# Kernel optimization log

Hardware: AMD Instinct MI355X
Metric: run time of the kernel (lower is better)

The kernel has to match this reference:

```python
import jax, jax.numpy as jnp
import numpy as np
from functools import partial

INPUT_SIZE = 24
HIDDEN = 64
NUM_LAYERS = 3
OUT_FEATURES = 4


def _lstm_layer(x, w_ih, w_hh, b_ih, b_hh):
    """Single LSTM layer, PyTorch gate order (i, f, g, o).
    x: [B, T, in] -> returns h sequence [B, T, H]."""
    B = x.shape[0]
    H = w_hh.shape[1]
    # Precompute input contribution for all timesteps: [B, T, 4H]
    gx = jnp.einsum('bti,gi->btg', x, w_ih) + b_ih + b_hh

    def step(carry, g_t):
        h, c = carry
        gates = g_t + h @ w_hh.T  # [B, 4H]
        i, f, g, o = jnp.split(gates, 4, axis=-1)
        i = jax.nn.sigmoid(i)
        f = jax.nn.sigmoid(f)
        g = jnp.tanh(g)
        o = jax.nn.sigmoid(o)
        c = f * c + i * g
        h = o * jnp.tanh(c)
        return (h, c), h

    h0 = jnp.zeros((B, H), dtype=x.dtype)
    c0 = jnp.zeros((B, H), dtype=x.dtype)
    (_, _), hs = jax.lax.scan(step, (h0, c0), jnp.swapaxes(gx, 0, 1))  # hs: [T, B, H]
    return jnp.swapaxes(hs, 0, 1)  # [B, T, H]


def setup_inputs() -> dict:
    key = jax.random.key(0)
    ks = jax.random.split(key, 16)
    B, T = 1024, 512
    inp = {"x": jax.random.normal(ks[0], (B, T, INPUT_SIZE), dtype=jnp.float32)}
    k = 1
    s = 1.0 / np.sqrt(HIDDEN)
    for layer in range(NUM_LAYERS):
        in_dim = INPUT_SIZE if layer == 0 else HIDDEN
        inp[f"w_ih_{layer}"] = jax.random.uniform(ks[k], (4 * HIDDEN, in_dim), minval=-s, maxval=s, dtype=jnp.float32); k += 1
        inp[f"w_hh_{layer}"] = jax.random.uniform(ks[k], (4 * HIDDEN, HIDDEN), minval=-s, maxval=s, dtype=jnp.float32); k += 1
        inp[f"b_ih_{layer}"] = jax.random.uniform(ks[k], (4 * HIDDEN,), minval=-s, maxval=s, dtype=jnp.float32); k += 1
        inp[f"b_hh_{layer}"] = jax.random.uniform(ks[k], (4 * HIDDEN,), minval=-s, maxval=s, dtype=jnp.float32); k += 1
    inp["w_lin"] = jax.random.uniform(ks[13], (OUT_FEATURES, HIDDEN), minval=-s, maxval=s, dtype=jnp.float32)
    inp["b_lin"] = jax.random.uniform(ks[14], (OUT_FEATURES,), minval=-s, maxval=s, dtype=jnp.float32)
    return inp


def reference(x, w_ih_0, w_hh_0, b_ih_0, b_hh_0,
              w_ih_1, w_hh_1, b_ih_1, b_hh_1,
              w_ih_2, w_hh_2, b_ih_2, b_hh_2,
              w_lin, b_lin):
    params = [(w_ih_0, w_hh_0, b_ih_0, b_hh_0),
              (w_ih_1, w_hh_1, b_ih_1, b_hh_1),
              (w_ih_2, w_hh_2, b_ih_2, b_hh_2)]
    h = x
    for (w_ih, w_hh, b_ih, b_hh) in params:  # fixed 3-layer stack
        h = _lstm_layer(h, w_ih, w_hh, b_ih, b_hh)
    last = h[:, -1]                      # [B, H]
    return last @ w_lin.T + b_lin        # [B, 4]
```

## Files before the change

### kernel.cpp

```cpp
#include <hip/hip_runtime.h>


typedef __attribute__((ext_vector_type(8))) _Float16 half8;
typedef __attribute__((ext_vector_type(4))) float floatx4;

static constexpr int T_STEPS = 512;

#define NL2E  (-1.4426950408889634f)
#define N2L2E (-2.8853900817779268f)

#define H_OFF0   0
#define H_OFF1   1024
#define H_OFF2   2048
#define SM_BYTES 3072

__device__ __forceinline__ floatx4 mfma16(half8 a, half8 b, floatx4 c) {
    return __builtin_amdgcn_mfma_f32_16x16x32_f16(a, b, c, 0, 0, 0);
}

__device__ __forceinline__ half8 cvt8s(const float* src, float s) {
    float4 v0 = *(const float4*)(src);
    float4 v1 = *(const float4*)(src + 4);
    half8 h;
    h[0] = (_Float16)(v0.x * s); h[1] = (_Float16)(v0.y * s);
    h[2] = (_Float16)(v0.z * s); h[3] = (_Float16)(v0.w * s);
    h[4] = (_Float16)(v1.x * s); h[5] = (_Float16)(v1.y * s);
    h[6] = (_Float16)(v1.z * s); h[7] = (_Float16)(v1.w * s);
    return h;
}

__device__ __forceinline__ void lds_barrier() {
    asm volatile("s_waitcnt lgkmcnt(0)" ::: "memory");
    __builtin_amdgcn_s_barrier();
}

__global__ __launch_bounds__(768, 3) void lstm3_v12(
    const float* __restrict__ x,
    const float* __restrict__ w_ih0, const float* __restrict__ w_hh0,
    const float* __restrict__ b_ih0, const float* __restrict__ b_hh0,
    const float* __restrict__ w_ih1, const float* __restrict__ w_hh1,
    const float* __restrict__ b_ih1, const float* __restrict__ b_hh1,
    const float* __restrict__ w_ih2, const float* __restrict__ w_hh2,
    const float* __restrict__ b_ih2, const float* __restrict__ b_hh2,
    const float* __restrict__ w_lin, const float* __restrict__ b_lin,
    float* __restrict__ out)
{
    __shared__ __align__(16) char sm[SM_BYTES];

    const int tid  = threadIdx.x;
    const int lane = tid & 63;
    const int wave = tid >> 6;
    const int L    = wave >> 2;
    const int w    = wave & 3;
    const int l15  = lane & 15;
    const int l4   = lane >> 4;
    const int bat  = l15 >> 2;
    const int b0   = blockIdx.x * 4;
    const int u    = w * 16 + l15;

    for (int i = tid; i < SM_BYTES / 16; i += 768)
        *(floatx4*)(&sm[i * 16]) = floatx4{0.f, 0.f, 0.f, 0.f};

    const float* wi = (L == 0) ? w_ih0 : (L == 1 ? w_ih1 : w_ih2);
    const float* wh = (L == 0) ? w_hh0 : (L == 1 ? w_hh1 : w_hh2);
    const float* bi = (L == 0) ? b_ih0 : (L == 1 ? b_ih1 : b_ih2);
    const float* bh = (L == 0) ? b_hh0 : (L == 1 ? b_hh1 : b_hh2);
    const int HB = (L == 0) ? H_OFF0 : (L == 1 ? H_OFF1 : H_OFF2);
    const int PB = (L == 1) ? H_OFF0 : H_OFF1;

    half8 wf[4][4];
#pragma unroll
    for (int tt = 0; tt < 4; ++tt) {
        const int g = tt * 64 + u;
        const float sc = (tt == 2) ? N2L2E : NL2E;
        if (L == 0) {
            half8 z;
#pragma unroll
            for (int j = 0; j < 8; ++j) z[j] = (_Float16)0.f;
            wf[tt][0] = (l4 < 3) ? cvt8s(w_ih0 + g * 24 + l4 * 8, sc) : z;
            wf[tt][1] = cvt8s(w_hh0 + g * 64 + l4 * 8, sc);
            wf[tt][2] = cvt8s(w_hh0 + g * 64 + 32 + l4 * 8, sc);
            wf[tt][3] = z;
        } else {
            wf[tt][0] = cvt8s(wi + g * 64 + l4 * 8, sc);
            wf[tt][1] = cvt8s(wi + g * 64 + 32 + l4 * 8, sc);
            wf[tt][2] = cvt8s(wh + g * 64 + l4 * 8, sc);
            wf[tt][3] = cvt8s(wh + g * 64 + 32 + l4 * 8, sc);
        }
    }
    floatx4 bv[4];
#pragma unroll
    for (int tt = 0; tt < 4; ++tt) {
        const float sc = (tt == 2) ? N2L2E : NL2E;
        float b = sc * (bi[tt * 64 + u] + bh[tt * 64 + u]);
        bv[tt][0] = b; bv[tt][1] = b; bv[tt][2] = b; bv[tt][3] = b;
    }
    const floatx4 Z4 = floatx4{0.f, 0.f, 0.f, 0.f};

    const int swzR = (bat & 1) << 5;
    int rb0 = 0, rb1 = 0, rb2 = 0, rb3 = 0;
    if (L == 0) {
        rb1 = H_OFF0 + ((bat * 128 + 0  + l4 * 16) ^ swzR);
        rb2 = H_OFF0 + ((bat * 128 + 64 + l4 * 16) ^ swzR);
    } else {
        rb0 = PB + ((bat * 128 + 0  + l4 * 16) ^ swzR);
        rb1 = PB + ((bat * 128 + 64 + l4 * 16) ^ swzR);
        rb2 = HB + ((bat * 128 + 0  + l4 * 16) ^ swzR);
        rb3 = HB + ((bat * 128 + 64 + l4 * 16) ^ swzR);
    }
    const int wb = HB + ((l4 * 128 + u * 2) ^ ((l4 & 1) << 5));

    const int par_e = L & 1;
    const int so_e = par_e * 512, sp_e = (par_e ^ 1) * 512;
    const int eA0 = rb0 + so_e;
    const int eA1 = rb1 + ((L == 0) ? sp_e : so_e);
    const int eA2 = rb2 + sp_e;
    const int eA3 = rb3 + sp_e;
    const int eWr = wb + so_e;
    const int oA0 = rb0 + sp_e;
    const int oA1 = rb1 + ((L == 0) ? so_e : sp_e);
    const int oA2 = rb2 + so_e;
    const int oA3 = rb3 + so_e;
    const int oWr = wb + sp_e;

    float4 xA0{0,0,0,0}, xA1{0,0,0,0}, xB0{0,0,0,0}, xB1{0,0,0,0};
    const bool xv = (L == 0) && (l4 < 3);
    const float* xpe = nullptr;
    const float* xpo = nullptr;
    if (xv) {
        const float* xb_ = x + (long)(b0 + bat) * T_STEPS * 24 + l4 * 8;
        xA0 = *(const float4*)(xb_);      xA1 = *(const float4*)(xb_ + 4);
        xB0 = *(const float4*)(xb_ + 24); xB1 = *(const float4*)(xb_ + 28);
        xpe = xb_ + 48;
        xpo = xb_ + 72;
    }

    float cst = 0.0f;
    __syncthreads();

    auto body = [&](int s, int A0, int A1, int A2, int A3, int WR)
        __attribute__((always_inline)) {
        const int t = s - L;
        const bool active = ((unsigned)t < (unsigned)T_STEPS);

        if (active) {
            float e0, e1, e2, e3;
            if (L == 0) {
                const float4 v0 = (t & 1) ? xB0 : xA0;
                const float4 v1 = (t & 1) ? xB1 : xA1;
                half8 aX;
                aX[0] = (_Float16)v0.x; aX[1] = (_Float16)v0.y;
                aX[2] = (_Float16)v0.z; aX[3] = (_Float16)v0.w;
                aX[4] = (_Float16)v1.x; aX[5] = (_Float16)v1.y;
                aX[6] = (_Float16)v1.z; aX[7] = (_Float16)v1.w;
                half8 a1 = *(const half8*)(&sm[A1]);
                half8 a2 = *(const half8*)(&sm[A2]);
#pragma unroll
                for (int tt = 0; tt < 4; ++tt) {
                    floatx4 accA = mfma16(aX, wf[tt][0], bv[tt]);
                    floatx4 accB = mfma16(a1, wf[tt][1], Z4);
                    accB = mfma16(a2, wf[tt][2], accB);
                    float e = __builtin_amdgcn_exp2f(accA[0] + accB[0]);
                    if (tt == 0) e0 = e; else if (tt == 1) e1 = e;
                    else if (tt == 2) e2 = e; else e3 = e;
                }
                if (xv && t + 2 < T_STEPS) {
                    if (t & 1) {
                        xB0 = *(const float4*)(xpo); xB1 = *(const float4*)(xpo + 4);
                        xpo += 48;
                    } else {
                        xA0 = *(const float4*)(xpe); xA1 = *(const float4*)(xpe + 4);
                        xpe += 48;
                    }
                }
            } else {
                half8 a0 = *(const half8*)(&sm[A0]);
                half8 a1 = *(const half8*)(&sm[A1]);
                half8 a2 = *(const half8*)(&sm[A2]);
                half8 a3 = *(const half8*)(&sm[A3]);
#pragma unroll
                for (int tt = 0; tt < 4; ++tt) {
                    floatx4 accA = mfma16(a0, wf[tt][0], bv[tt]);
                    floatx4 accB = mfma16(a2, wf[tt][2], Z4);
                    accA = mfma16(a1, wf[tt][1], accA);
                    accB = mfma16(a3, wf[tt][3], accB);
                    float e = __builtin_amdgcn_exp2f(accA[0] + accB[0]);
                    if (tt == 0) e0 = e; else if (tt == 1) e1 = e;
                    else if (tt == 2) e2 = e; else e3 = e;
                }
            }

            float ig = __builtin_amdgcn_rcpf(1.f + e0);
            float fg = __builtin_amdgcn_rcpf(1.f + e1);
            float sg = __builtin_amdgcn_rcpf(1.f + e2);
            float og = __builtin_amdgcn_rcpf(1.f + e3);
            float gg = fmaf(2.f, sg, -1.f);
            cst = fmaf(fg, cst, ig * gg);
            float et = __builtin_amdgcn_exp2f(cst * N2L2E);
            float th = fmaf(2.f, __builtin_amdgcn_rcpf(1.f + et), -1.f);
            float hv = og * th;
            *(_Float16*)(&sm[WR]) = (_Float16)hv;
        }
        lds_barrier();
    };

    for (int s = 0; s < T_STEPS + 2; s += 2) {
        body(s,     eA0, eA1, eA2, eA3, eWr);
        body(s + 1, oA0, oA1, oA2, oA3, oWr);
    }

    __syncthreads();

    if (tid < 16) {
        const int bb = tid >> 2, o = tid & 3;
        const int sl = ((T_STEPS - 1) & 1) * 512;
        float accum = b_lin[o];
#pragma unroll
        for (int k = 0; k < 64; ++k) {
            const int off = H_OFF2 + sl + ((bb * 128 + k * 2) ^ ((bb & 1) << 5));
            accum = fmaf((float)*(const _Float16*)(&sm[off]), w_lin[o * 64 + k], accum);
        }
        out[(b0 + bb) * 4 + o] = accum;
    }
}

extern "C" void kernel_launch(void* const* d_in, const int* in_sizes, int n_in,
                              void* d_out, int out_size, void* d_ws, size_t ws_size,
                              hipStream_t stream) {
    const float* x     = (const float*)d_in[0];
    const float* w_ih0 = (const float*)d_in[1];
    const float* w_hh0 = (const float*)d_in[2];
    const float* b_ih0 = (const float*)d_in[3];
    const float* b_hh0 = (const float*)d_in[4];
    const float* w_ih1 = (const float*)d_in[5];
    const float* w_hh1 = (const float*)d_in[6];
    const float* b_ih1 = (const float*)d_in[7];
    const float* b_hh1 = (const float*)d_in[8];
    const float* w_ih2 = (const float*)d_in[9];
    const float* w_hh2 = (const float*)d_in[10];
    const float* b_ih2 = (const float*)d_in[11];
    const float* b_hh2 = (const float*)d_in[12];
    const float* w_lin = (const float*)d_in[13];
    const float* b_lin = (const float*)d_in[14];

    lstm3_v12<<<dim3(256), dim3(768), 0, stream>>>(
        x, w_ih0, w_hh0, b_ih0, b_hh0,
        w_ih1, w_hh1, b_ih1, b_hh1,
        w_ih2, w_hh2, b_ih2, b_hh2,
        w_lin, b_lin, (float*)d_out);
}
```

Baseline: 310.2 us.

## Stage layer-0 inputs through double-buffered LDS and chain MFMA accumulators

Layer-0 input rows are now loaded cooperatively by a few lanes per wave, one timestep ahead, converted to fp16 and written into a double-buffered LDS region. The MFMA loop then reads a ready half8 operand instead of each lane holding its own float registers and converting them every step. This removes redundant per-lane global loads and conversions and frees registers. Separately, the split dual-accumulator MFMA chains are merged into one serial chain, which saves a vector add but lengthens the MFMA dependency chain.

```diff
diff --git a/kernel.cpp b/kernel.cpp
--- a/kernel.cpp
+++ b/kernel.cpp
@@ -2,6 +2,7 @@
 
 
 typedef __attribute__((ext_vector_type(8))) _Float16 half8;
+typedef __attribute__((ext_vector_type(4))) _Float16 half4;
 typedef __attribute__((ext_vector_type(4))) float floatx4;
 
 static constexpr int T_STEPS = 512;
@@ -9,10 +10,11 @@
 #define NL2E  (-1.4426950408889634f)
 #define N2L2E (-2.8853900817779268f)
 
-#define H_OFF0   0
-#define H_OFF1   1024
-#define H_OFF2   2048
-#define SM_BYTES 3072
+#define XOFF     0
+#define H_OFF0   512
+#define H_OFF1   1536
+#define H_OFF2   2560
+#define SM_BYTES 3584
 
 __device__ __forceinline__ floatx4 mfma16(half8 a, half8 b, floatx4 c) {
     return __builtin_amdgcn_mfma_f32_16x16x32_f16(a, b, c, 0, 0, 0);
@@ -34,7 +36,7 @@
     __builtin_amdgcn_s_barrier();
 }
 
-__global__ __launch_bounds__(768, 3) void lstm3_v12(
+__global__ __launch_bounds__(768, 3) void lstm3_v13(
     const float* __restrict__ x,
     const float* __restrict__ w_ih0, const float* __restrict__ w_hh0,
     const float* __restrict__ b_ih0, const float* __restrict__ b_hh0,
@@ -95,7 +97,6 @@
         float b = sc * (bi[tt * 64 + u] + bh[tt * 64 + u]);
         bv[tt][0] = b; bv[tt][1] = b; bv[tt][2] = b; bv[tt][3] = b;
     }
-    const floatx4 Z4 = floatx4{0.f, 0.f, 0.f, 0.f};
 
     const int swzR = (bat & 1) << 5;
     int rb0 = 0, rb1 = 0, rb2 = 0, rb3 = 0;
@@ -109,6 +110,9 @@
         rb3 = HB + ((bat * 128 + 64 + l4 * 16) ^ swzR);
     }
     const int wb = HB + ((l4 * 128 + u * 2) ^ ((l4 & 1) << 5));
+
+    const int xr0 = XOFF + bat * 64 + l4 * 16;
+    const int xr1 = xr0 + 256;
 
     const int par_e = L & 1;
     const int so_e = par_e * 512, sp_e = (par_e ^ 1) * 512;
@@ -123,55 +127,46 @@
     const int oA3 = rb3 + so_e;
     const int oWr = wb + sp_e;
 
-    float4 xA0{0,0,0,0}, xA1{0,0,0,0}, xB0{0,0,0,0}, xB1{0,0,0,0};
-    const bool xv = (L == 0) && (l4 < 3);
-    const float* xpe = nullptr;
-    const float* xpo = nullptr;
-    if (xv) {
-        const float* xb_ = x + (long)(b0 + bat) * T_STEPS * 24 + l4 * 8;
-        xA0 = *(const float4*)(xb_);      xA1 = *(const float4*)(xb_ + 4);
-        xB0 = *(const float4*)(xb_ + 24); xB1 = *(const float4*)(xb_ + 28);
-        xpe = xb_ + 48;
-        xpo = xb_ + 72;
+    const bool stg = (L == 0) && (lane < 6);
+    const int xf = lane;
+    const int sxw0 = XOFF + 0   + w * 64 + xf * 8;
+    const int sxw1 = XOFF + 256 + w * 64 + xf * 8;
+    const float* xg = nullptr;
+    if (stg) xg = x + ((long)(b0 + w) * T_STEPS + 1) * 24 + xf * 4;
+
+    if (stg) {
+        float4 v = *(const float4*)(x + ((long)(b0 + w) * T_STEPS + 0) * 24 + xf * 4);
+        half4 hv; hv[0] = (_Float16)v.x; hv[1] = (_Float16)v.y;
+                  hv[2] = (_Float16)v.z; hv[3] = (_Float16)v.w;
+        *(half4*)(&sm[sxw0]) = hv;
     }
 
     float cst = 0.0f;
     __syncthreads();
 
-    auto body = [&](int s, int A0, int A1, int A2, int A3, int WR)
-        __attribute__((always_inline)) {
+    auto body = [&](int s, int A0, int A1, int A2, int A3, int WR,
+                    int XR, int SXW) __attribute__((always_inline)) {
         const int t = s - L;
         const bool active = ((unsigned)t < (unsigned)T_STEPS);
+
+        float4 xld;
+        const bool do_x = stg && (s + 1 < T_STEPS);
+        if (do_x) xld = *(const float4*)xg;
 
         if (active) {
             float e0, e1, e2, e3;
             if (L == 0) {
-                const float4 v0 = (t & 1) ? xB0 : xA0;
-                const float4 v1 = (t & 1) ? xB1 : xA1;
-                half8 aX;
-                aX[0] = (_Float16)v0.x; aX[1] = (_Float16)v0.y;
-                aX[2] = (_Float16)v0.z; aX[3] = (_Float16)v0.w;
-                aX[4] = (_Float16)v1.x; aX[5] = (_Float16)v1.y;
-                aX[6] = (_Float16)v1.z; aX[7] = (_Float16)v1.w;
+                half8 aX = *(const half8*)(&sm[XR]);
                 half8 a1 = *(const half8*)(&sm[A1]);
                 half8 a2 = *(const half8*)(&sm[A2]);
 #pragma unroll
                 for (int tt = 0; tt < 4; ++tt) {
-                    floatx4 accA = mfma16(aX, wf[tt][0], bv[tt]);
-                    floatx4 accB = mfma16(a1, wf[tt][1], Z4);
-                    accB = mfma16(a2, wf[tt][2], accB);
-                    float e = __builtin_amdgcn_exp2f(accA[0] + accB[0]);
+                    floatx4 acc = mfma16(aX, wf[tt][0], bv[tt]);
+                    acc = mfma16(a1, wf[tt][1], acc);
+                    acc = mfma16(a2, wf[tt][2], acc);
+                    float e = __builtin_amdgcn_exp2f(acc[0]);
                     if (tt == 0) e0 = e; else if (tt == 1) e1 = e;
                     else if (tt == 2) e2 = e; else e3 = e;
-                }
-                if (xv && t + 2 < T_STEPS) {
-                    if (t & 1) {
-                        xB0 = *(const float4*)(xpo); xB1 = *(const float4*)(xpo + 4);
-                        xpo += 48;
-                    } else {
-                        xA0 = *(const float4*)(xpe); xA1 = *(const float4*)(xpe + 4);
-                        xpe += 48;
-                    }
                 }
             } else {
                 half8 a0 = *(const half8*)(&sm[A0]);
@@ -180,11 +175,11 @@
                 half8 a3 = *(const half8*)(&sm[A3]);
 #pragma unroll
                 for (int tt = 0; tt < 4; ++tt) {
-                    floatx4 accA = mfma16(a0, wf[tt][0], bv[tt]);
-                    floatx4 accB = mfma16(a2, wf[tt][2], Z4);
-                    accA = mfma16(a1, wf[tt][1], accA);
-                    accB = mfma16(a3, wf[tt][3], accB);
-                    float e = __builtin_amdgcn_exp2f(accA[0] + accB[0]);
+                    floatx4 acc = mfma16(a0, wf[tt][0], bv[tt]);
+                    acc = mfma16(a1, wf[tt][1], acc);
+                    acc = mfma16(a2, wf[tt][2], acc);
+                    acc = mfma16(a3, wf[tt][3], acc);
+                    float e = __builtin_amdgcn_exp2f(acc[0]);
                     if (tt == 0) e0 = e; else if (tt == 1) e1 = e;
                     else if (tt == 2) e2 = e; else e3 = e;
                 }
@@ -201,12 +196,19 @@
             float hv = og * th;
             *(_Float16*)(&sm[WR]) = (_Float16)hv;
         }
+
+        if (do_x) {
+            half4 hv; hv[0] = (_Float16)xld.x; hv[1] = (_Float16)xld.y;
+                      hv[2] = (_Float16)xld.z; hv[3] = (_Float16)xld.w;
+            *(half4*)(&sm[SXW]) = hv;
+            xg += 24;
+        }
         lds_barrier();
     };
 
     for (int s = 0; s < T_STEPS + 2; s += 2) {
-        body(s,     eA0, eA1, eA2, eA3, eWr);
-        body(s + 1, oA0, oA1, oA2, oA3, oWr);
+        body(s,     eA0, eA1, eA2, eA3, eWr, xr0, sxw1);
+        body(s + 1, oA0, oA1, oA2, oA3, oWr, xr1, sxw0);
     }
 
     __syncthreads();
@@ -243,7 +245,7 @@
     const float* w_lin = (const float*)d_in[13];
     const float* b_lin = (const float*)d_in[14];
 
-    lstm3_v12<<<dim3(256), dim3(768), 0, stream>>>(
+    lstm3_v13<<<dim3(256), dim3(768), 0, stream>>>(
         x, w_ih0, w_hh0, b_ih0, b_hh0,
         w_ih1, w_hh1, b_ih1, b_hh1,
         w_ih2, w_hh2, b_ih2, b_hh2,
```

New measurement: 327.3 us. 5.5% more time.
